# Optimization experiments

Measured on AMD Instinct MI355X. Metric: run time of the kernel, lower is better.

The kernel has to match this reference:

```python
import jax, jax.numpy as jnp
import numpy as np

B, T, TR, DIM, H = 1, 4096, 1024, 1536, 12
DH = DIM // H          # 128
EPS = 1e-6             # RMSNorm eps
REF_SCALE = 1.0


def setup_inputs() -> dict:
    key = jax.random.key(0)
    ks = jax.random.split(key, 20)
    s = 0.02
    w = lambda k: jax.random.normal(k, (DIM, DIM), jnp.float32) * s
    b = lambda k: jax.random.normal(k, (DIM,), jnp.float32) * 0.01
    theta = jax.random.uniform(ks[2], (T, DH // 2), jnp.float32) * (2.0 * np.pi)
    return {
        "hidden_states": jax.random.normal(ks[0], (B, T, DIM), jnp.float32),
        "ref_hidden_states": jax.random.normal(ks[1], (B, TR, DIM), jnp.float32),
        "rot_cos": jnp.cos(theta),
        "rot_sin": jnp.sin(theta),
        "Wq": w(ks[3]), "bq": b(ks[4]),
        "Wk": w(ks[5]), "bk": b(ks[6]),
        "Wv": w(ks[7]), "bv": b(ks[8]),
        "Wkr": w(ks[9]), "bkr": b(ks[10]),
        "Wvr": w(ks[11]), "bvr": b(ks[12]),
        "Wo": w(ks[13]), "bo": b(ks[14]),
        "gq": jnp.ones((DIM,), jnp.float32),
        "gk": jnp.ones((DIM,), jnp.float32),
    }


def _rmsnorm(x, g):
    return x * jax.lax.rsqrt(jnp.mean(x * x, axis=-1, keepdims=True) + EPS) * g


def _heads(x):  # [B, T, DIM] -> [B, H, T, DH]
    return x.reshape(B, -1, H, DH).transpose(0, 2, 1, 3)


def _merge(x):  # [B, H, T, DH] -> [B, T, DIM]
    return x.transpose(0, 2, 1, 3).reshape(B, -1, DIM)


def _rope(x, c, s):
    # consecutive pairs along DH form complex numbers (view_as_complex semantics)
    xe, xo = x[..., 0::2], x[..., 1::2]
    c = c[None, None]  # [1,1,T,DH/2]
    s = s[None, None]
    re = xe * c - xo * s
    im = xe * s + xo * c
    return jnp.stack([re, im], axis=-1).reshape(x.shape)


def _attn(q, k, v):
    scale = 1.0 / jnp.sqrt(jnp.asarray(DH, q.dtype))
    p = jax.nn.softmax(jnp.einsum("bhqd,bhkd->bhqk", q, k) * scale, axis=-1)
    return jnp.einsum("bhqk,bhkd->bhqd", p, v)


def reference(hidden_states, ref_hidden_states, rot_cos, rot_sin,
              Wq, bq, Wk, bk, Wv, bv, Wkr, bkr, Wvr, bvr, Wo, bo, gq, gk):
    # QKV projections (self-attention: encoder_hidden_states = hidden_states)
    q_lin = hidden_states @ Wq + bq
    k_lin = hidden_states @ Wk + bk
    v_lin = hidden_states @ Wv + bv

    # ---- reference-attention branch (uses pre-RoPE query) ----
    ref_q = _heads(_rmsnorm(q_lin, gq))
    ref_k = _heads(_rmsnorm(ref_hidden_states @ Wkr + bkr, gk))
    ref_v = _heads(ref_hidden_states @ Wvr + bvr)
    ref_out = _merge(_attn(ref_q, ref_k, ref_v))  # [B, T, DIM]

    # ---- main attention with QK-norm + RoPE ----
    q = _rope(_heads(_rmsnorm(q_lin, gq)), rot_cos, rot_sin)
    k = _rope(_heads(_rmsnorm(k_lin, gk)), rot_cos, rot_sin)
    v = _heads(v_lin)
    main_out = _merge(_attn(q, k, v))  # [B, T, DIM]

    # scaled residual combine + output projection (dropout = identity)
    out = main_out + REF_SCALE * ref_out
    return out @ Wo + bo
```

## Files before the change

### kernel.cpp

```cpp
#include <hip/hip_runtime.h>

typedef unsigned short u16;
typedef unsigned int u32;
typedef __attribute__((ext_vector_type(8))) short short8;
typedef __attribute__((ext_vector_type(4))) float f32x4;

__device__ inline u16 f2b(float f) {
  u32 u = __builtin_bit_cast(u32, f);
  u += 0x7fff + ((u >> 16) & 1);
  return (u16)(u >> 16);
}
__device__ inline float b2f(u16 u) {
  return __builtin_bit_cast(float, (u32)u << 16);
}
__device__ inline u32 pack_bf16_rn(float a, float b) {
  const u32 ua = __builtin_bit_cast(u32, a) + 0x8000u;
  const u32 ub = __builtin_bit_cast(u32, b) + 0x8000u;
  return (ua >> 16) | (ub & 0xffff0000u);
}
__device__ inline void c_store(float* p, float v) { *p = v; }
__device__ inline void c_store(u16* p, float v) { *p = f2b(v); }

__device__ inline float fexp2(float x) {
#if __has_builtin(__builtin_amdgcn_exp2f)
  return __builtin_amdgcn_exp2f(x);
#else
  return exp2f(x);
#endif
}

typedef const __attribute__((address_space(1))) u32 gu32;
typedef __attribute__((address_space(3))) u32 lu32;
__device__ inline void async16(const u16* g, u16* l) {
  __builtin_amdgcn_global_load_lds((gu32*)g, (lu32*)l, 16, 0, 0);
}

#define QS (0.08838834764831843f * 1.4426950408889634f)

template <int MI, typename TC>
__global__ __launch_bounds__(256) void gemm128_kernel(
    const u16* __restrict__ A, long lda,
    const u16* __restrict__ Bt, long ldb,
    TC* __restrict__ C0, TC* __restrict__ C1, TC* __restrict__ C2, long ldc,
    const float* b0, const float* b1, const float* b2,
    int K) {
  __shared__ u16 As[32 * MI * 32];
  __shared__ u16 Bs[128 * 32];

  const int tid = threadIdx.x;
  const int lane = tid & 63;
  const int w = tid >> 6;
  const int r = lane & 15;
  const int quad = lane >> 4;
  const int m0 = blockIdx.y * (32 * MI);
  const int nb = blockIdx.x * 128;
  const int seg = nb / 1536;
  const int nc = nb - seg * 1536;
  TC* C = seg == 0 ? C0 : (seg == 1 ? C1 : C2);
  const float* bias = seg == 0 ? b0 : (seg == 1 ? b1 : b2);

  const int srow = lane >> 2;
  const int sx = ((lane & 3) ^ (srow & 3)) * 8;
  const u16* Ag = A + (size_t)(m0 + w * 8 * MI + srow) * lda + sx;
  const u16* Bg = Bt + (size_t)(nb + w * 32 + srow) * ldb + sx;
  u16* Al[MI / 2];
#pragma unroll
  for (int j = 0; j < MI / 2; ++j) Al[j] = &As[(w * 8 * MI + 16 * j) * 32];
  u16* const Bl0 = &Bs[(w * 32) * 32];
  u16* const Bl1 = &Bs[(w * 32 + 16) * 32];

  const int wm = (w >> 1) * (16 * MI);
  const int wn = (w & 1) * 64;

  f32x4 acc[MI][4];
#pragma unroll
  for (int i = 0; i < MI; ++i)
#pragma unroll
    for (int j = 0; j < 4; ++j) acc[i][j] = (f32x4){0.f, 0.f, 0.f, 0.f};

  const int fco = (quad ^ (r & 3)) * 8;

  for (int kk = 0; kk < K; kk += 32) {
    __syncthreads();
#pragma unroll
    for (int j = 0; j < MI / 2; ++j) async16(Ag + kk + (size_t)(16 * j) * lda, Al[j]);
    async16(Bg + kk, Bl0);
    async16(Bg + kk + 16 * ldb, Bl1);
    __syncthreads();

    short8 af[MI], bf[4];
#pragma unroll
    for (int mi = 0; mi < MI; ++mi)
      af[mi] = *reinterpret_cast<const short8*>(&As[(wm + 16 * mi + r) * 32 + fco]);
#pragma unroll
    for (int ni = 0; ni < 4; ++ni)
      bf[ni] = *reinterpret_cast<const short8*>(&Bs[(wn + 16 * ni + r) * 32 + fco]);
#pragma unroll
    for (int mi = 0; mi < MI; ++mi)
#pragma unroll
      for (int ni = 0; ni < 4; ++ni)
        acc[mi][ni] = __builtin_amdgcn_mfma_f32_16x16x32_bf16(af[mi], bf[ni], acc[mi][ni], 0, 0, 0);
  }

#pragma unroll
  for (int mi = 0; mi < MI; ++mi)
#pragma unroll
    for (int ni = 0; ni < 4; ++ni)
#pragma unroll
      for (int rr = 0; rr < 4; ++rr) {
        const int row = m0 + wm + 16 * mi + 4 * quad + rr;
        const int col = nc + wn + 16 * ni + r;
        c_store(&C[(size_t)row * ldc + col], acc[mi][ni][rr] + bias[col]);
      }
}

__global__ __launch_bounds__(256) void conv2_kernel(
    const float* __restrict__ xa, u16* __restrict__ ya, int n8a,
    const float* __restrict__ xb, u16* __restrict__ yb, int n8b) {
  int i = blockIdx.x * 256 + threadIdx.x;
  const float* x;
  u16* y;
  if (i < n8a) {
    x = xa; y = ya;
  } else {
    i -= n8a;
    if (i >= n8b) return;
    x = xb; y = yb;
  }
  const float4 v0 = reinterpret_cast<const float4*>(x)[2 * i];
  const float4 v1 = reinterpret_cast<const float4*>(x)[2 * i + 1];
  uint4 rv;
  rv.x = (u32)f2b(v0.x) | ((u32)f2b(v0.y) << 16);
  rv.y = (u32)f2b(v0.z) | ((u32)f2b(v0.w) << 16);
  rv.z = (u32)f2b(v1.x) | ((u32)f2b(v1.y) << 16);
  rv.w = (u32)f2b(v1.z) | ((u32)f2b(v1.w) << 16);
  reinterpret_cast<uint4*>(y)[i] = rv;
}

__device__ inline void transconv_body(const float* __restrict__ W, u16* __restrict__ Wt) {
  __shared__ u16 Ls[64 * 72];
  const int tid = threadIdx.x;
  const int k0 = blockIdx.y * 64;
  const int n0 = blockIdx.x * 64;
#pragma unroll
  for (int i = 0; i < 4; ++i) {
    const int c = tid + 256 * i;
    const int row = c >> 4;
    const int c4 = (c & 15) * 4;
    const float4 v = *reinterpret_cast<const float4*>(&W[(size_t)(k0 + row) * 1536 + n0 + c4]);
    Ls[(c4 + 0) * 72 + row] = f2b(v.x);
    Ls[(c4 + 1) * 72 + row] = f2b(v.y);
    Ls[(c4 + 2) * 72 + row] = f2b(v.z);
    Ls[(c4 + 3) * 72 + row] = f2b(v.w);
  }
  __syncthreads();
#pragma unroll
  for (int i = 0; i < 2; ++i) {
    const int c = tid + 256 * i;
    const int n = c >> 3;
    const int kc = (c & 7) * 8;
    u16 tmp[8];
#pragma unroll
    for (int j = 0; j < 8; ++j) tmp[j] = Ls[n * 72 + kc + j];
    *reinterpret_cast<uint4*>(&Wt[(size_t)(n0 + n) * 1536 + k0 + kc]) =
        *reinterpret_cast<const uint4*>(tmp);
  }
}

__global__ __launch_bounds__(256) void transconv6_kernel(
    const float* W0, const float* W1, const float* W2,
    const float* W3, const float* W4, const float* W5,
    u16* T0, u16* T1, u16* T2, u16* T3, u16* T4, u16* T5) {
  const int z = blockIdx.z;
  const float* W = z == 0 ? W0 : z == 1 ? W1 : z == 2 ? W2 : z == 3 ? W3 : z == 4 ? W4 : W5;
  u16* Wt = z == 0 ? T0 : z == 1 ? T1 : z == 2 ? T2 : z == 3 ? T3 : z == 4 ? T4 : T5;
  transconv_body(W, Wt);
}

__global__ __launch_bounds__(256) void rmsnorm3_kernel(
    const u16* xq, const u16* xk, const u16* xkr,
    const float* gq, const float* gk,
    const float* rc, const float* rs,
    u16* oq_plain, u16* oq_rope, u16* ok_rope, u16* okr_plain) {
  __shared__ float red[4];
  const int z = blockIdx.y;
  const int row = blockIdx.x;
  if (z == 2 && row >= 1024) return;
  const u16* x; const float* g; u16* po; u16* pr; float sc;
  if (z == 0)      { x = xq;  g = gq; po = oq_plain; pr = oq_rope; sc = QS;  }
  else if (z == 1) { x = xk;  g = gk; po = nullptr;  pr = ok_rope; sc = 1.f; }
  else             { x = xkr; g = gk; po = okr_plain; pr = nullptr; sc = 1.f; }

  const int tid = threadIdx.x;
  const u32* xr = reinterpret_cast<const u32*>(x + (size_t)row * 1536);
  float xe[3], xo[3];
  float ss = 0.f;
#pragma unroll
  for (int j = 0; j < 3; ++j) {
    const u32 u = xr[tid + 256 * j];
    const float e = b2f((u16)(u & 0xffff));
    const float o = b2f((u16)(u >> 16));
    xe[j] = e; xo[j] = o;
    ss += e * e + o * o;
  }
#pragma unroll
  for (int off = 32; off; off >>= 1) ss += __shfl_xor(ss, off, 64);
  if ((tid & 63) == 0) red[tid >> 6] = ss;
  __syncthreads();
  const float total = red[0] + red[1] + red[2] + red[3];
  const float rinv = rsqrtf(total * (1.0f / 1536.0f) + 1e-6f) * sc;
  u32* po32 = po ? reinterpret_cast<u32*>(po + (size_t)row * 1536) : nullptr;
  u32* pr32 = pr ? reinterpret_cast<u32*>(pr + (size_t)row * 1536) : nullptr;
#pragma unroll
  for (int j = 0; j < 3; ++j) {
    const int p = tid + 256 * j;
    const float2 gg = reinterpret_cast<const float2*>(g)[p];
    const float e = xe[j] * rinv * gg.x;
    const float o = xo[j] * rinv * gg.y;
    if (po32) po32[p] = (u32)f2b(e) | ((u32)f2b(o) << 16);
    if (pr32) {
      const int i = p & 63;
      const float c = rc[row * 64 + i];
      const float s = rs[row * 64 + i];
      const float re = e * c - o * s;
      const float im = e * s + o * c;
      pr32[p] = (u32)f2b(re) | ((u32)f2b(im) << 16);
    }
  }
}

__global__ __launch_bounds__(256) void vtrans2_kernel(
    const u16* __restrict__ V0, u16* __restrict__ Vt0,
    const u16* __restrict__ V1, u16* __restrict__ Vt1) {
  __shared__ u16 Ls[64 * 136];
  const int z = blockIdx.z;
  const int kvLen = z == 0 ? 4096 : 1024;
  const int kv0 = blockIdx.x * 64;
  if (kv0 >= kvLen) return;
  const u16* V = z == 0 ? V0 : V1;
  u16* Vt = z == 0 ? Vt0 : Vt1;
  const int tid = threadIdx.x;
  const int h = blockIdx.y;
#pragma unroll
  for (int i = 0; i < 4; ++i) {
    const int c = tid + 256 * i;
    const int row = c >> 4, c8 = c & 15;
    *reinterpret_cast<uint4*>(&Ls[row * 136 + 8 * c8]) =
        *reinterpret_cast<const uint4*>(V + (size_t)(kv0 + row) * 1536 + h * 128 + 8 * c8);
  }
  __syncthreads();
#pragma unroll
  for (int i = 0; i < 4; ++i) {
    const int c = tid + 256 * i;
    const int d = c >> 3, kc = c & 7;
    u16 tmp[8];
#pragma unroll
    for (int j = 0; j < 8; ++j) tmp[j] = Ls[(8 * kc + j) * 136 + d];
    *reinterpret_cast<uint4*>(Vt + ((size_t)h * 128 + d) * kvLen + kv0 + 8 * kc) =
        *reinterpret_cast<const uint4*>(tmp);
  }
}

__global__ __launch_bounds__(128, 2) void flash_kernel(
    const u16* __restrict__ Qc, const u16* __restrict__ Kc,
    const u16* __restrict__ Vc, int kvLenC,
    const u16* __restrict__ Qm, const u16* __restrict__ Km,
    const u16* __restrict__ Vm, int kvLenM,
    float* __restrict__ O, u16* __restrict__ Ob) {
  __shared__ u16 Ks[2][32 * 128];
  __shared__ u16 Vs[2][128 * 32];
  __shared__ u16 Pb[2][32 * 40];
  __shared__ float ab[4][16];

  const int tid = threadIdx.x;
  const int lane = tid & 63;
  const int w = tid >> 6;
  const int r = lane & 15;
  const int quad = lane >> 4;
  const int h = blockIdx.y;
  const int q0 = blockIdx.x * 64;
  const int fv = (r >> 1) & 3;

  auto run_pass = [&](const u16* __restrict__ Q, const u16* __restrict__ K,
                      const u16* __restrict__ Vt, int kvLen, bool addO) {
    short8 qf[2][4];
#pragma unroll
    for (int qt = 0; qt < 2; ++qt) {
      const u16* qbase = Q + (size_t)(q0 + 32 * w + 16 * qt + r) * 1536 + h * 128 + 8 * quad;
#pragma unroll
      for (int ks = 0; ks < 4; ++ks)
        qf[qt][ks] = *reinterpret_cast<const short8*>(qbase + 32 * ks);
    }

    const u16* Kb = K + h * 128;
    const u16* Vb = Vt + (size_t)h * 128 * kvLen;
    u32 koff[4], voff[4];
    int klo[4], vlo[4];
    {
      const int p16 = lane & 15, rin = lane >> 4;
      const int p4 = lane & 3, din = lane >> 2;
#pragma unroll
      for (int j = 0; j < 4; ++j) {
        const int row = 16 * w + 4 * j + rin;
        koff[j] = (u32)row * 1536u + 8u * (u32)(p16 ^ (row & 15));
        klo[j] = (16 * w + 4 * j) * 128;
        const int d = 64 * w + 16 * j + din;
        voff[j] = (u32)d * (u32)kvLen + 8u * (u32)(p4 ^ ((d >> 1) & 3));
        vlo[j] = (64 * w + 16 * j) * 32;
      }
    }

    f32x4 Oc[2][8];
#pragma unroll
    for (int qt = 0; qt < 2; ++qt)
#pragma unroll
      for (int dt = 0; dt < 8; ++dt) Oc[qt][dt] = (f32x4){0.f, 0.f, 0.f, 0.f};
    float m_i[2] = {-1e30f, -1e30f}, l_i[2] = {0.f, 0.f};

    const int nt = kvLen >> 5;

#pragma unroll
    for (int j = 0; j < 4; ++j) async16(Kb + koff[j], &Ks[0][klo[j]]);
#pragma unroll
    for (int j = 0; j < 4; ++j) async16(Vb + voff[j], &Vs[0][vlo[j]]);

    for (int t = 0; t < nt; ++t) {
      const int buf = t & 1;
      __syncthreads();
      if (t + 1 < nt) {
        const size_t ko = (size_t)(t + 1) * (32 * 1536);
        const size_t vo = (size_t)(t + 1) * 32;
#pragma unroll
        for (int j = 0; j < 4; ++j) async16(Kb + ko + koff[j], &Ks[buf ^ 1][klo[j]]);
#pragma unroll
        for (int j = 0; j < 4; ++j) async16(Vb + vo + voff[j], &Vs[buf ^ 1][vlo[j]]);
      }

      f32x4 St[2][2];
#pragma unroll
      for (int qt = 0; qt < 2; ++qt)
#pragma unroll
        for (int mt = 0; mt < 2; ++mt) St[qt][mt] = (f32x4){0.f, 0.f, 0.f, 0.f};
      __builtin_amdgcn_s_setprio(1);
#pragma unroll
      for (int mt = 0; mt < 2; ++mt) {
        const u16* kp = &Ks[buf][(16 * mt + r) * 128];
#pragma unroll
        for (int ks = 0; ks < 4; ++ks) {
          const short8 af = *reinterpret_cast<const short8*>(kp + 8 * ((quad + 4 * ks) ^ r));
#pragma unroll
          for (int qt = 0; qt < 2; ++qt)
            St[qt][mt] = __builtin_amdgcn_mfma_f32_16x16x32_bf16(af, qf[qt][ks], St[qt][mt], 0, 0, 0);
        }
      }
      __builtin_amdgcn_s_setprio(0);

      uint2 pk[2][2];
#pragma unroll
      for (int qt = 0; qt < 2; ++qt) {
        float mloc = -1e30f;
#pragma unroll
        for (int mt = 0; mt < 2; ++mt)
#pragma unroll
          for (int rr = 0; rr < 4; ++rr) mloc = fmaxf(mloc, St[qt][mt][rr]);
        mloc = fmaxf(mloc, __shfl_xor(mloc, 16, 64));
        mloc = fmaxf(mloc, __shfl_xor(mloc, 32, 64));

        float alpha = 1.0f;
        if (__any(mloc > m_i[qt] + 11.5f)) {
          const float mn = fmaxf(m_i[qt], mloc);
          alpha = fexp2(m_i[qt] - mn);
          m_i[qt] = mn;
          if (quad == 0) ab[2 * w + qt][r] = alpha;
          const float4 a4 = *reinterpret_cast<const float4*>(&ab[2 * w + qt][4 * quad]);
#pragma unroll
          for (int dt = 0; dt < 8; ++dt) {
            Oc[qt][dt][0] *= a4.x; Oc[qt][dt][1] *= a4.y;
            Oc[qt][dt][2] *= a4.z; Oc[qt][dt][3] *= a4.w;
          }
        }

        float psum = 0.f;
#pragma unroll
        for (int mt = 0; mt < 2; ++mt) {
          const float p0 = fexp2(St[qt][mt][0] - m_i[qt]);
          const float p1 = fexp2(St[qt][mt][1] - m_i[qt]);
          const float p2 = fexp2(St[qt][mt][2] - m_i[qt]);
          const float p3 = fexp2(St[qt][mt][3] - m_i[qt]);
          psum += (p0 + p1) + (p2 + p3);
          pk[qt][mt].x = pack_bf16_rn(p0, p1);
          pk[qt][mt].y = pack_bf16_rn(p2, p3);
        }
        psum += __shfl_xor(psum, 16, 64);
        psum += __shfl_xor(psum, 32, 64);
        l_i[qt] = l_i[qt] * alpha + psum;
      }

#pragma unroll
      for (int qt = 0; qt < 2; ++qt)
#pragma unroll
        for (int mt = 0; mt < 2; ++mt)
          *reinterpret_cast<uint2*>(&Pb[w][(16 * qt + r) * 40 + 16 * mt + 4 * quad]) = pk[qt][mt];
      {
        short8 pa[2];
#pragma unroll
        for (int qt = 0; qt < 2; ++qt)
          pa[qt] = *reinterpret_cast<const short8*>(&Pb[w][(16 * qt + r) * 40 + 8 * quad]);
        __builtin_amdgcn_s_setprio(1);
#pragma unroll
        for (int dt = 0; dt < 8; ++dt) {
          const int d = 16 * dt + r;
          const short8 b0 = *reinterpret_cast<const short8*>(&Vs[buf][d * 32 + 8 * (quad ^ fv)]);
#pragma unroll
          for (int qt = 0; qt < 2; ++qt)
            Oc[qt][dt] = __builtin_amdgcn_mfma_f32_16x16x32_bf16(pa[qt], b0, Oc[qt][dt], 0, 0, 0);
        }
        __builtin_amdgcn_s_setprio(0);
      }
    }

#pragma unroll
    for (int qt = 0; qt < 2; ++qt) {
      if (quad == 0) ab[2 * w + qt][r] = 1.0f / l_i[qt];
      const float4 li4 = *reinterpret_cast<const float4*>(&ab[2 * w + qt][4 * quad]);
      const float lv[4] = {li4.x, li4.y, li4.z, li4.w};
      const int rowb = q0 + 32 * w + 16 * qt;
      float* obf = O + (size_t)rowb * 1536 + h * 128;
      u16* obb = Ob + (size_t)rowb * 1536 + h * 128;
#pragma unroll
      for (int rr = 0; rr < 4; ++rr) {
        float* orow = obf + (size_t)(4 * quad + rr) * 1536 + r;
        u16* brow = obb + (size_t)(4 * quad + rr) * 1536 + r;
#pragma unroll
        for (int dt = 0; dt < 8; ++dt) {
          float v = Oc[qt][dt][rr] * lv[rr];
          if (addO) {
            v += orow[16 * dt];
            brow[16 * dt] = f2b(v);
          } else {
            orow[16 * dt] = v;
          }
        }
      }
    }
  };

  run_pass(Qc, Kc, Vc, kvLenC, false);
  __syncthreads();
  run_pass(Qm, Km, Vm, kvLenM, true);
}

extern "C" void kernel_launch(void* const* d_in, const int* in_sizes, int n_in,
                              void* d_out, int out_size, void* d_ws, size_t ws_size,
                              hipStream_t stream) {
  (void)in_sizes; (void)n_in; (void)out_size; (void)ws_size;
  constexpr int T = 4096, TR = 1024, DIM = 1536, NH = 12;

  const float* hs  = (const float*)d_in[0];
  const float* rhs = (const float*)d_in[1];
  const float* rc  = (const float*)d_in[2];
  const float* rs  = (const float*)d_in[3];
  const float* Wq  = (const float*)d_in[4];
  const float* bq  = (const float*)d_in[5];
  const float* Wk  = (const float*)d_in[6];
  const float* bk  = (const float*)d_in[7];
  const float* Wv  = (const float*)d_in[8];
  const float* bv  = (const float*)d_in[9];
  const float* Wkr = (const float*)d_in[10];
  const float* bkr = (const float*)d_in[11];
  const float* Wvr = (const float*)d_in[12];
  const float* bvr = (const float*)d_in[13];
  const float* Wo  = (const float*)d_in[14];
  const float* bo  = (const float*)d_in[15];
  const float* gq  = (const float*)d_in[16];
  const float* gk  = (const float*)d_in[17];
  float* out = (float*)d_out;

  char* ws = (char*)d_ws;
  size_t off = 0;
  auto alloc = [&](size_t bytes) -> void* {
    void* p = ws + off;
    off += (bytes + 255) & ~(size_t)255;
    return p;
  };
  u16* bQ    = (u16*)alloc((size_t)T * DIM * 2);
  u16* bQr   = (u16*)alloc((size_t)T * DIM * 2);
  u16* bK    = (u16*)alloc((size_t)T * DIM * 2);
  u16* bV    = (u16*)alloc((size_t)T * DIM * 2);
  u16* bKr   = (u16*)alloc((size_t)TR * DIM * 2);
  u16* bVr   = (u16*)alloc((size_t)TR * DIM * 2);
  float* bO  = (float*)alloc((size_t)T * DIM * 4);
  u16* bHs   = (u16*)alloc((size_t)T * DIM * 2);
  u16* bRhs  = (u16*)alloc((size_t)TR * DIM * 2);
  u16* bWqkv = (u16*)alloc((size_t)3 * DIM * DIM * 2);
  u16* bWr   = (u16*)alloc((size_t)2 * DIM * DIM * 2);
  u16* bWoT  = (u16*)alloc((size_t)DIM * DIM * 2);
  u16* VtG = bHs;
  u16* VtR = bRhs;
  u16* bOb = bWqkv;

  const dim3 blk(256);

  conv2_kernel<<<dim3((T * DIM / 8 + TR * DIM / 8 + 255) / 256), blk, 0, stream>>>(
      hs, bHs, T * DIM / 8, rhs, bRhs, TR * DIM / 8);

  transconv6_kernel<<<dim3(24, 24, 6), blk, 0, stream>>>(
      Wq, Wk, Wv, Wkr, Wvr, Wo,
      bWqkv + 0 * (size_t)DIM * DIM, bWqkv + 1 * (size_t)DIM * DIM,
      bWqkv + 2 * (size_t)DIM * DIM, bWr + 0 * (size_t)DIM * DIM,
      bWr + 1 * (size_t)DIM * DIM, bWoT);

  gemm128_kernel<4, u16><<<dim3(36, 32), blk, 0, stream>>>(
      bHs, DIM, bWqkv, DIM, bQ, bK, bV, DIM, bq, bk, bv, DIM);
  gemm128_kernel<2, u16><<<dim3(24, 16), blk, 0, stream>>>(
      bRhs, DIM, bWr, DIM, bKr, bVr, (u16*)nullptr, DIM, bkr, bvr, nullptr, DIM);

  rmsnorm3_kernel<<<dim3(T, 3), blk, 0, stream>>>(
      bQ, bK, bKr, gq, gk, rc, rs, bQ, bQr, bK, bKr);

  vtrans2_kernel<<<dim3(T / 64, NH, 2), blk, 0, stream>>>(bV, VtG, bVr, VtR);

  flash_kernel<<<dim3(T / 64, NH), dim3(128), 0, stream>>>(
      bQ, bKr, VtR, TR, bQr, bK, VtG, T, bO, bOb);

  gemm128_kernel<2, float><<<dim3(12, 64), blk, 0, stream>>>(
      bOb, DIM, bWoT, DIM, out, (float*)nullptr, (float*)nullptr, DIM, bo, nullptr, nullptr, DIM);
}
```

Baseline: 581.7 us.

## Split flash attention KV tiles across wave pairs with split-softmax merge

```diff
diff --git a/kernel.cpp b/kernel.cpp
--- a/kernel.cpp
+++ b/kernel.cpp
@@ -3,6 +3,8 @@
 typedef unsigned short u16;
 typedef unsigned int u32;
 typedef __attribute__((ext_vector_type(8))) short short8;
+typedef __attribute__((ext_vector_type(4))) short s16x4;
+typedef __attribute__((ext_vector_type(2))) u32 u32x2;
 typedef __attribute__((ext_vector_type(4))) float f32x4;
 
 __device__ inline u16 f2b(float f) {
@@ -26,6 +28,16 @@
   return __builtin_amdgcn_exp2f(x);
 #else
   return exp2f(x);
+#endif
+}
+
+__device__ inline f32x4 mfma16x16x16(s16x4 a, s16x4 b, f32x4 c) {
+#if __has_builtin(__builtin_amdgcn_mfma_f32_16x16x16bf16_1k)
+  return __builtin_amdgcn_mfma_f32_16x16x16bf16_1k(a, b, c, 0, 0, 0);
+#else
+  const short8 a8 = {a[0], a[1], a[2], a[3], 0, 0, 0, 0};
+  const short8 b8 = {b[0], b[1], b[2], b[3], 0, 0, 0, 0};
+  return __builtin_amdgcn_mfma_f32_16x16x32_bf16(a8, b8, c, 0, 0, 0);
 #endif
 }
 
@@ -44,8 +56,8 @@
     TC* __restrict__ C0, TC* __restrict__ C1, TC* __restrict__ C2, long ldc,
     const float* b0, const float* b1, const float* b2,
     int K) {
-  __shared__ u16 As[32 * MI * 32];
-  __shared__ u16 Bs[128 * 32];
+  __shared__ __align__(16) u16 As[32 * MI * 32];
+  __shared__ __align__(16) u16 Bs[128 * 32];
 
   const int tid = threadIdx.x;
   const int lane = tid & 63;
@@ -138,7 +150,7 @@
 }
 
 __device__ inline void transconv_body(const float* __restrict__ W, u16* __restrict__ Wt) {
-  __shared__ u16 Ls[64 * 72];
+  __shared__ __align__(16) u16 Ls[64 * 72];
   const int tid = threadIdx.x;
   const int k0 = blockIdx.y * 64;
   const int n0 = blockIdx.x * 64;
@@ -232,7 +244,7 @@
 __global__ __launch_bounds__(256) void vtrans2_kernel(
     const u16* __restrict__ V0, u16* __restrict__ Vt0,
     const u16* __restrict__ V1, u16* __restrict__ Vt1) {
-  __shared__ u16 Ls[64 * 136];
+  __shared__ __align__(16) u16 Ls[64 * 136];
   const int z = blockIdx.z;
   const int kvLen = z == 0 ? 4096 : 1024;
   const int kv0 = blockIdx.x * 64;
@@ -261,32 +273,36 @@
   }
 }
 
-__global__ __launch_bounds__(128, 2) void flash_kernel(
+__global__ __launch_bounds__(256, 3) void flash_kernel(
     const u16* __restrict__ Qc, const u16* __restrict__ Kc,
     const u16* __restrict__ Vc, int kvLenC,
     const u16* __restrict__ Qm, const u16* __restrict__ Km,
     const u16* __restrict__ Vm, int kvLenM,
     float* __restrict__ O, u16* __restrict__ Ob) {
-  __shared__ u16 Ks[2][32 * 128];
-  __shared__ u16 Vs[2][128 * 32];
-  __shared__ u16 Pb[2][32 * 40];
-  __shared__ float ab[4][16];
+  __shared__ __align__(16) u16 Ka[2][32 * 128];
+  __shared__ __align__(16) u16 Va[2][128 * 32];
+  __shared__ __align__(16) float ab[4][2][16];
+  __shared__ __align__(16) float ab0[2][2][16];
+  __shared__ __align__(16) float2 mlb[2][2][16];
 
   const int tid = threadIdx.x;
   const int lane = tid & 63;
   const int w = tid >> 6;
+  const int p = w >> 1;
+  const int qh = w & 1;
   const int r = lane & 15;
   const int quad = lane >> 4;
   const int h = blockIdx.y;
   const int q0 = blockIdx.x * 64;
-  const int fv = (r >> 1) & 3;
 
   auto run_pass = [&](const u16* __restrict__ Q, const u16* __restrict__ K,
                       const u16* __restrict__ Vt, int kvLen, bool addO) {
+    __syncthreads();
+
     short8 qf[2][4];
 #pragma unroll
     for (int qt = 0; qt < 2; ++qt) {
-      const u16* qbase = Q + (size_t)(q0 + 32 * w + 16 * qt + r) * 1536 + h * 128 + 8 * quad;
+      const u16* qbase = Q + (size_t)(q0 + 32 * qh + 16 * qt + r) * 1536 + h * 128 + 8 * quad;
 #pragma unroll
       for (int ks = 0; ks < 4; ++ks)
         qf[qt][ks] = *reinterpret_cast<const short8*>(qbase + 32 * ks);
@@ -294,19 +310,19 @@
 
     const u16* Kb = K + h * 128;
     const u16* Vb = Vt + (size_t)h * 128 * kvLen;
-    u32 koff[4], voff[4];
-    int klo[4], vlo[4];
+    u32 koff[2], voff[2];
+    int klo[2], vlo[2];
     {
       const int p16 = lane & 15, rin = lane >> 4;
       const int p4 = lane & 3, din = lane >> 2;
 #pragma unroll
-      for (int j = 0; j < 4; ++j) {
-        const int row = 16 * w + 4 * j + rin;
+      for (int j = 0; j < 2; ++j) {
+        const int row = 8 * w + 4 * j + rin;
         koff[j] = (u32)row * 1536u + 8u * (u32)(p16 ^ (row & 15));
-        klo[j] = (16 * w + 4 * j) * 128;
-        const int d = 64 * w + 16 * j + din;
-        voff[j] = (u32)d * (u32)kvLen + 8u * (u32)(p4 ^ ((d >> 1) & 3));
-        vlo[j] = (64 * w + 16 * j) * 32;
+        klo[j] = (8 * w + 4 * j) * 128;
+        const int d = 32 * w + 16 * j + din;
+        voff[j] = (u32)d * (u32)kvLen + 8u * (u32)(p4 ^ ((din >> 1) & 3));
+        vlo[j] = (32 * w + 16 * j) * 32;
       }
     }
 
@@ -320,9 +336,9 @@
     const int nt = kvLen >> 5;
 
 #pragma unroll
-    for (int j = 0; j < 4; ++j) async16(Kb + koff[j], &Ks[0][klo[j]]);
-#pragma unroll
-    for (int j = 0; j < 4; ++j) async16(Vb + voff[j], &Vs[0][vlo[j]]);
+    for (int j = 0; j < 2; ++j) async16(Kb + koff[j], &Ka[0][klo[j]]);
+#pragma unroll
+    for (int j = 0; j < 2; ++j) async16(Vb + voff[j], &Va[0][vlo[j]]);
 
     for (int t = 0; t < nt; ++t) {
       const int buf = t & 1;
@@ -331,114 +347,120 @@
         const size_t ko = (size_t)(t + 1) * (32 * 1536);
         const size_t vo = (size_t)(t + 1) * 32;
 #pragma unroll
-        for (int j = 0; j < 4; ++j) async16(Kb + ko + koff[j], &Ks[buf ^ 1][klo[j]]);
-#pragma unroll
-        for (int j = 0; j < 4; ++j) async16(Vb + vo + voff[j], &Vs[buf ^ 1][vlo[j]]);
-      }
-
-      f32x4 St[2][2];
-#pragma unroll
-      for (int qt = 0; qt < 2; ++qt)
-#pragma unroll
-        for (int mt = 0; mt < 2; ++mt) St[qt][mt] = (f32x4){0.f, 0.f, 0.f, 0.f};
+        for (int j = 0; j < 2; ++j) async16(Kb + ko + koff[j], &Ka[buf ^ 1][klo[j]]);
+#pragma unroll
+        for (int j = 0; j < 2; ++j) async16(Vb + vo + voff[j], &Va[buf ^ 1][vlo[j]]);
+      }
+
+      const u16* kp = &Ka[buf][(16 * p + r) * 128];
+      short8 af[4];
+#pragma unroll
+      for (int ks = 0; ks < 4; ++ks)
+        af[ks] = *reinterpret_cast<const short8*>(kp + 8 * ((quad + 4 * ks) ^ r));
+      f32x4 St[2];
+#pragma unroll
+      for (int qt = 0; qt < 2; ++qt) St[qt] = (f32x4){0.f, 0.f, 0.f, 0.f};
       __builtin_amdgcn_s_setprio(1);
 #pragma unroll
-      for (int mt = 0; mt < 2; ++mt) {
-        const u16* kp = &Ks[buf][(16 * mt + r) * 128];
-#pragma unroll
-        for (int ks = 0; ks < 4; ++ks) {
-          const short8 af = *reinterpret_cast<const short8*>(kp + 8 * ((quad + 4 * ks) ^ r));
-#pragma unroll
-          for (int qt = 0; qt < 2; ++qt)
-            St[qt][mt] = __builtin_amdgcn_mfma_f32_16x16x32_bf16(af, qf[qt][ks], St[qt][mt], 0, 0, 0);
-        }
-      }
+      for (int ks = 0; ks < 4; ++ks)
+#pragma unroll
+        for (int qt = 0; qt < 2; ++qt)
+          St[qt] = __builtin_amdgcn_mfma_f32_16x16x32_bf16(af[ks], qf[qt][ks], St[qt], 0, 0, 0);
       __builtin_amdgcn_s_setprio(0);
 
-      uint2 pk[2][2];
+      s16x4 pa[2];
 #pragma unroll
       for (int qt = 0; qt < 2; ++qt) {
-        float mloc = -1e30f;
-#pragma unroll
-        for (int mt = 0; mt < 2; ++mt)
-#pragma unroll
-          for (int rr = 0; rr < 4; ++rr) mloc = fmaxf(mloc, St[qt][mt][rr]);
+        float mloc = fmaxf(fmaxf(St[qt][0], St[qt][1]), fmaxf(St[qt][2], St[qt][3]));
         mloc = fmaxf(mloc, __shfl_xor(mloc, 16, 64));
         mloc = fmaxf(mloc, __shfl_xor(mloc, 32, 64));
-
         float alpha = 1.0f;
         if (__any(mloc > m_i[qt] + 11.5f)) {
           const float mn = fmaxf(m_i[qt], mloc);
           alpha = fexp2(m_i[qt] - mn);
           m_i[qt] = mn;
-          if (quad == 0) ab[2 * w + qt][r] = alpha;
-          const float4 a4 = *reinterpret_cast<const float4*>(&ab[2 * w + qt][4 * quad]);
+          if (quad == 0) ab[w][qt][r] = alpha;
+          const float4 a4 = *reinterpret_cast<const float4*>(&ab[w][qt][4 * quad]);
 #pragma unroll
           for (int dt = 0; dt < 8; ++dt) {
             Oc[qt][dt][0] *= a4.x; Oc[qt][dt][1] *= a4.y;
             Oc[qt][dt][2] *= a4.z; Oc[qt][dt][3] *= a4.w;
           }
         }
-
-        float psum = 0.f;
-#pragma unroll
-        for (int mt = 0; mt < 2; ++mt) {
-          const float p0 = fexp2(St[qt][mt][0] - m_i[qt]);
-          const float p1 = fexp2(St[qt][mt][1] - m_i[qt]);
-          const float p2 = fexp2(St[qt][mt][2] - m_i[qt]);
-          const float p3 = fexp2(St[qt][mt][3] - m_i[qt]);
-          psum += (p0 + p1) + (p2 + p3);
-          pk[qt][mt].x = pack_bf16_rn(p0, p1);
-          pk[qt][mt].y = pack_bf16_rn(p2, p3);
-        }
+        const float p0 = fexp2(St[qt][0] - m_i[qt]);
+        const float p1 = fexp2(St[qt][1] - m_i[qt]);
+        const float p2 = fexp2(St[qt][2] - m_i[qt]);
+        const float p3 = fexp2(St[qt][3] - m_i[qt]);
+        float psum = (p0 + p1) + (p2 + p3);
         psum += __shfl_xor(psum, 16, 64);
         psum += __shfl_xor(psum, 32, 64);
         l_i[qt] = l_i[qt] * alpha + psum;
-      }
-
+        pa[qt] = __builtin_bit_cast(s16x4, (u32x2){pack_bf16_rn(p0, p1), pack_bf16_rn(p2, p3)});
+      }
+
+      s16x4 vf[8];
+#pragma unroll
+      for (int dt = 0; dt < 8; ++dt) {
+        const int d = 16 * dt + r;
+        const int cst = (2 * p + (quad >> 1)) ^ ((r >> 1) & 3);
+        vf[dt] = *reinterpret_cast<const s16x4*>(&Va[buf][d * 32 + 8 * cst + 4 * (quad & 1)]);
+      }
+      __builtin_amdgcn_s_setprio(1);
+#pragma unroll
+      for (int dt = 0; dt < 8; ++dt)
+#pragma unroll
+        for (int qt = 0; qt < 2; ++qt)
+          Oc[qt][dt] = mfma16x16x16(pa[qt], vf[dt], Oc[qt][dt]);
+      __builtin_amdgcn_s_setprio(0);
+    }
+
+    __syncthreads();
+    float* sc = (qh == 0) ? reinterpret_cast<float*>(&Ka[0][0])
+                          : reinterpret_cast<float*>(&Va[0][0]);
+    if (p == 0) {
+      if (quad == 0) {
+#pragma unroll
+        for (int qt = 0; qt < 2; ++qt) mlb[qh][qt][r] = (float2){m_i[qt], l_i[qt]};
+      }
 #pragma unroll
       for (int qt = 0; qt < 2; ++qt)
 #pragma unroll
-        for (int mt = 0; mt < 2; ++mt)
-          *reinterpret_cast<uint2*>(&Pb[w][(16 * qt + r) * 40 + 16 * mt + 4 * quad]) = pk[qt][mt];
-      {
-        short8 pa[2];
-#pragma unroll
-        for (int qt = 0; qt < 2; ++qt)
-          pa[qt] = *reinterpret_cast<const short8*>(&Pb[w][(16 * qt + r) * 40 + 8 * quad]);
-        __builtin_amdgcn_s_setprio(1);
-#pragma unroll
-        for (int dt = 0; dt < 8; ++dt) {
-          const int d = 16 * dt + r;
-          const short8 b0 = *reinterpret_cast<const short8*>(&Vs[buf][d * 32 + 8 * (quad ^ fv)]);
-#pragma unroll
-          for (int qt = 0; qt < 2; ++qt)
-            Oc[qt][dt] = __builtin_amdgcn_mfma_f32_16x16x32_bf16(pa[qt], b0, Oc[qt][dt], 0, 0, 0);
-        }
-        __builtin_amdgcn_s_setprio(0);
-      }
+        for (int dt = 0; dt < 8; ++dt)
+#pragma unroll
+          for (int rr = 0; rr < 4; ++rr)
+            sc[(16 * qt + 4 * quad + rr) * 128 + 16 * dt + r] = Oc[qt][dt][rr];
     }
-
-#pragma unroll
-    for (int qt = 0; qt < 2; ++qt) {
-      if (quad == 0) ab[2 * w + qt][r] = 1.0f / l_i[qt];
-      const float4 li4 = *reinterpret_cast<const float4*>(&ab[2 * w + qt][4 * quad]);
-      const float lv[4] = {li4.x, li4.y, li4.z, li4.w};
-      const int rowb = q0 + 32 * w + 16 * qt;
-      float* obf = O + (size_t)rowb * 1536 + h * 128;
-      u16* obb = Ob + (size_t)rowb * 1536 + h * 128;
-#pragma unroll
-      for (int rr = 0; rr < 4; ++rr) {
-        float* orow = obf + (size_t)(4 * quad + rr) * 1536 + r;
-        u16* brow = obb + (size_t)(4 * quad + rr) * 1536 + r;
-#pragma unroll
-        for (int dt = 0; dt < 8; ++dt) {
-          float v = Oc[qt][dt][rr] * lv[rr];
-          if (addO) {
-            v += orow[16 * dt];
-            brow[16 * dt] = f2b(v);
-          } else {
-            orow[16 * dt] = v;
+    __syncthreads();
+    if (p == 1) {
+#pragma unroll
+      for (int qt = 0; qt < 2; ++qt) {
+        const float2 ml0 = mlb[qh][qt][r];
+        const float m = fmaxf(ml0.x, m_i[qt]);
+        const float s0 = fexp2(ml0.x - m), s1 = fexp2(m_i[qt] - m);
+        const float rinv = 1.0f / (ml0.y * s0 + l_i[qt] * s1);
+        if (quad == 0) { ab[w][qt][r] = s1 * rinv; ab0[qh][qt][r] = s0 * rinv; }
+      }
+#pragma unroll
+      for (int qt = 0; qt < 2; ++qt) {
+        const float4 a1 = *reinterpret_cast<const float4*>(&ab[w][qt][4 * quad]);
+        const float4 a0 = *reinterpret_cast<const float4*>(&ab0[qh][qt][4 * quad]);
+        const float a1v[4] = {a1.x, a1.y, a1.z, a1.w};
+        const float a0v[4] = {a0.x, a0.y, a0.z, a0.w};
+        const int rowb = q0 + 32 * qh + 16 * qt;
+#pragma unroll
+        for (int rr = 0; rr < 4; ++rr) {
+          float* orow = O + (size_t)(rowb + 4 * quad + rr) * 1536 + h * 128 + r;
+          u16* brow = Ob + (size_t)(rowb + 4 * quad + rr) * 1536 + h * 128 + r;
+#pragma unroll
+          for (int dt = 0; dt < 8; ++dt) {
+            const float o0 = sc[(16 * qt + 4 * quad + rr) * 128 + 16 * dt + r];
+            float v = Oc[qt][dt][rr] * a1v[rr] + o0 * a0v[rr];
+            if (addO) {
+              v += orow[16 * dt];
+              brow[16 * dt] = f2b(v);
+            } else {
+              orow[16 * dt] = v;
+            }
           }
         }
       }
@@ -446,7 +468,6 @@
   };
 
   run_pass(Qc, Kc, Vc, kvLenC, false);
-  __syncthreads();
   run_pass(Qm, Km, Vm, kvLenM, true);
 }
 
@@ -520,7 +541,7 @@
 
   vtrans2_kernel<<<dim3(T / 64, NH, 2), blk, 0, stream>>>(bV, VtG, bVr, VtR);
 
-  flash_kernel<<<dim3(T / 64, NH), dim3(128), 0, stream>>>(
+  flash_kernel<<<dim3(T / 64, NH), blk, 0, stream>>>(
       bQ, bKr, VtR, TR, bQr, bK, VtG, T, bO, bOb);
 
   gemm128_kernel<2, float><<<dim3(12, 64), blk, 0, stream>>>(
```

Result: faster. 562.2 us (-3.3%).
